# Optimization experiments

Measured on AMD Instinct MI355X. Metric: run time of the kernel, lower is better.

Reference implementation:

```python
import jax, jax.numpy as jnp
import numpy as np

K = 5
THRESHOLD = 0.1


def _l2norm(x, eps=1e-12):
    # matches torch.nn.functional.normalize(dim=-1)
    n = jnp.sqrt(jnp.sum(x * x, axis=-1, keepdims=True))
    return x / jnp.maximum(n, eps)


def setup_inputs() -> dict:
    key = jax.random.key(0)
    ks = jax.random.split(key, 5)
    B, CDD, HIS, L, LVL, H = 32, 5, 50, 32, 2, 256
    return {
        "cdd_repr": jax.random.normal(ks[0], (B, CDD, H), dtype=jnp.float32),
        "his_repr": jax.random.normal(ks[1], (B, HIS, H), dtype=jnp.float32),
        "his_embedding": jax.random.normal(ks[2], (B, HIS, L, LVL, H), dtype=jnp.float32),
        "his_attn_mask": jax.random.randint(ks[3], (B, HIS, L), 0, 2).astype(jnp.int32),
        # xavier-normal-ish init for the selection projection
        "W": jax.random.normal(ks[4], (H, H), dtype=jnp.float32) * np.float32(np.sqrt(2.0 / (H + H))),
        "b": jnp.zeros((H,), dtype=jnp.float32),
    }


def reference(cdd_repr, his_repr, his_embedding, his_attn_mask, W, b):
    # selection projection + L2 normalize
    c = _l2norm(cdd_repr @ W.T + b)           # [B, cdd, H]
    h = _l2norm(his_repr @ W.T + b)           # [B, his, H]
    # news-level attention scores
    attn = jnp.einsum("bcd,bhd->bch", c, h)   # [B, cdd, his]
    # top-k history selection (sorted descending, like torch.topk)
    vals, idx = jax.lax.top_k(attn, K)        # [B, cdd, k]
    # gather top-k history embeddings / masks per (batch, cdd)
    his_activated = jax.vmap(lambda e, i: e[i])(his_embedding, idx)   # [B, cdd, k, L, lvl, H]
    his_mask_activated = jax.vmap(lambda m, i: m[i])(his_attn_mask, idx)  # [B, cdd, k, L]
    # threshold mask + reweight (fused elementwise)
    w = jnp.where(vals < THRESHOLD, jnp.float32(0.0), vals)
    his_activated = his_activated * w[..., None, None, None]
    return his_activated, his_mask_activated
```

## Files before the change

kernel.cpp:

```cpp
#include <hip/hip_runtime.h>
#include <hip/hip_bf16.h>

#define B_    32
#define CDD_  5
#define HIS_  50
#define L_    32
#define LVL_  2
#define H_    256
#define K_    5
#define NCDD  (B_*CDD_)
#define NHIS  (B_*HIS_)
#define NROWS (NCDD + NHIS)
#define SLAB  (L_*LVL_*H_)
#define OUT0  ((size_t)NCDD*K_*SLAB)

__global__ __launch_bounds__(256) void proj_norm_kernel(
    const float* __restrict__ cdd, const float* __restrict__ his,
    const float* __restrict__ Wm, const float* __restrict__ bias,
    float* __restrict__ Y)
{
    __shared__ float xs[4][H_];
    __shared__ float part[4][4];
    __shared__ float inv[4];
    const int t = threadIdx.x;
    const int r0 = blockIdx.x * 4;

    {
        int rr = t >> 6, cc = t & 63;
        int row = r0 + rr;
        const float* src = (row < NCDD) ? (cdd + (size_t)row * H_)
                                        : (his + (size_t)(row - NCDD) * H_);
        ((float4*)xs[rr])[cc] = ((const float4*)src)[cc];
    }
    __syncthreads();

    float a0 = 0.f, a1 = 0.f, a2 = 0.f, a3 = 0.f;
    const float4* wrow = (const float4*)(Wm + (size_t)t * H_);
    #pragma unroll 8
    for (int c = 0; c < H_ / 4; ++c) {
        float4 wv = wrow[c];
        float4 x0 = ((float4*)xs[0])[c];
        float4 x1 = ((float4*)xs[1])[c];
        float4 x2 = ((float4*)xs[2])[c];
        float4 x3 = ((float4*)xs[3])[c];
        a0 += wv.x*x0.x + wv.y*x0.y + wv.z*x0.z + wv.w*x0.w;
        a1 += wv.x*x1.x + wv.y*x1.y + wv.z*x1.z + wv.w*x1.w;
        a2 += wv.x*x2.x + wv.y*x2.y + wv.z*x2.z + wv.w*x2.w;
        a3 += wv.x*x3.x + wv.y*x3.y + wv.z*x3.z + wv.w*x3.w;
    }
    const float bt = bias[t];
    float y0 = a0 + bt, y1 = a1 + bt, y2 = a2 + bt, y3 = a3 + bt;

    const int wave = t >> 6, lane = t & 63;
    float s0 = y0*y0, s1 = y1*y1, s2 = y2*y2, s3 = y3*y3;
    #pragma unroll
    for (int off = 32; off; off >>= 1) {
        s0 += __shfl_down(s0, off);
        s1 += __shfl_down(s1, off);
        s2 += __shfl_down(s2, off);
        s3 += __shfl_down(s3, off);
    }
    if (lane == 0) { part[0][wave] = s0; part[1][wave] = s1;
                     part[2][wave] = s2; part[3][wave] = s3; }
    __syncthreads();
    if (t < 4) {
        float s = part[t][0] + part[t][1] + part[t][2] + part[t][3];
        inv[t] = 1.0f / fmaxf(sqrtf(s), 1e-12f);
    }
    __syncthreads();

    float* yr = Y + (size_t)r0 * H_ + t;
    yr[0 * H_] = y0 * inv[0];
    yr[1 * H_] = y1 * inv[1];
    yr[2 * H_] = y2 * inv[2];
    yr[3 * H_] = y3 * inv[3];
}

__global__ __launch_bounds__(256) void attn_topk_kernel(
    const float* __restrict__ Y, const int* __restrict__ mask,
    int* __restrict__ idx_ws, float* __restrict__ w_ws,
    float* __restrict__ mask_out)
{
    const int bc = blockIdx.x;
    const int b  = bc / CDD_;
    __shared__ float cs[H_];
    __shared__ float scores[HIS_];
    __shared__ int   sidx[K_];
    const int t = threadIdx.x;

    cs[t] = Y[(size_t)bc * H_ + t];
    __syncthreads();

    const int wave = t >> 6, lane = t & 63;
    for (int h = wave; h < HIS_; h += 4) {
        const float4* hv = (const float4*)(Y + (size_t)(NCDD + b * HIS_ + h) * H_);
        float4 x  = hv[lane];
        float4 c4 = ((float4*)cs)[lane];
        float p = x.x*c4.x + x.y*c4.y + x.z*c4.z + x.w*c4.w;
        #pragma unroll
        for (int off = 32; off; off >>= 1) p += __shfl_down(p, off);
        if (lane == 0) scores[h] = p;
    }
    __syncthreads();

    if (t == 0) {
        #pragma unroll
        for (int k = 0; k < K_; ++k) {
            float best = -1e30f; int bi = 0;
            for (int h = 0; h < HIS_; ++h)
                if (scores[h] > best) { best = scores[h]; bi = h; }
            scores[bi] = -1e30f;
            sidx[k] = bi;
            idx_ws[bc * K_ + k] = bi;
            w_ws[bc * K_ + k]   = (best < 0.1f) ? 0.0f : best;
        }
    }
    __syncthreads();

    if (t < K_ * L_) {
        int k = t / L_, l = t % L_;
        mask_out[((size_t)bc * K_ + k) * L_ + l] =
            (float)mask[((size_t)(b * HIS_ + sidx[k])) * L_ + l];
    }
}

__global__ __launch_bounds__(256) void gather_scale_kernel(
    const float* __restrict__ emb, const int* __restrict__ idx_ws,
    const float* __restrict__ w_ws, float* __restrict__ out)
{
    const int gb    = blockIdx.x;
    const int slice = gb & 7;
    const int bck   = gb >> 3;
    const int bc    = bck / K_;
    const int b     = bc / CDD_;
    const int i     = idx_ws[bck];
    const float w   = w_ws[bck];

    const float4* src = (const float4*)(emb + (size_t)(b * HIS_ + i) * SLAB);
    float4*       dst = (float4*)(out + (size_t)bck * SLAB);
    const int base = slice * 512 + threadIdx.x;

    float4 v0 = src[base];
    float4 v1 = src[base + 256];
    v0.x *= w; v0.y *= w; v0.z *= w; v0.w *= w;
    v1.x *= w; v1.y *= w; v1.z *= w; v1.w *= w;
    dst[base]       = v0;
    dst[base + 256] = v1;
}

extern "C" void kernel_launch(void* const* d_in, const int* in_sizes, int n_in,
                              void* d_out, int out_size, void* d_ws, size_t ws_size,
                              hipStream_t stream) {
    const float* cdd  = (const float*)d_in[0];
    const float* his  = (const float*)d_in[1];
    const float* emb  = (const float*)d_in[2];
    const int*   mask = (const int*)  d_in[3];
    const float* Wm   = (const float*)d_in[4];
    const float* bias = (const float*)d_in[5];
    float* out = (float*)d_out;

    float* Y      = (float*)d_ws;
    int*   idx_ws = (int*)  ((char*)d_ws + (size_t)NROWS*H_*4);
    float* w_ws   = (float*)((char*)d_ws + (size_t)NROWS*H_*4 + 800*4);

    proj_norm_kernel<<<NROWS / 4, 256, 0, stream>>>(cdd, his, Wm, bias, Y);
    attn_topk_kernel<<<NCDD, 256, 0, stream>>>(Y, mask, idx_ws, w_ws, out + OUT0);
    gather_scale_kernel<<<NCDD * K_ * 8, 256, 0, stream>>>(emb, idx_ws, w_ws, out);
}
```

Baseline: 196.0 us.

## Transpose W for coalesced projection, skip gather loads for zero weights, nontemporal stores

Adds a kernel that transposes W so the projection kernel reads coalesced float4 rows of W^T, with each wave computing two rows and normalizing them via in-wave xor shuffles, which removes the block-level reductions and barriers. The gather kernel now uses fewer blocks, each handling four float4s per thread. It skips reading the embedding when the threshold weight is zero and writes zeros instead. Output writes use nontemporal stores to avoid polluting cache. This adds an extra kernel launch for the transpose.

```diff
diff --git a/kernel.cpp b/kernel.cpp
--- a/kernel.cpp
+++ b/kernel.cpp
@@ -14,19 +14,36 @@
 #define SLAB  (L_*LVL_*H_)
 #define OUT0  ((size_t)NCDD*K_*SLAB)
 
+typedef float f32x4 __attribute__((ext_vector_type(4)));
+
+__global__ __launch_bounds__(256) void transpose_w_kernel(
+    const float* __restrict__ Wm, float* __restrict__ WT)
+{
+    __shared__ float tile[64][65];
+    const int tx = threadIdx.x & 63, ty = threadIdx.x >> 6;
+    const int c0 = (blockIdx.x & 3) * 64, r0 = (blockIdx.x >> 2) * 64;
+    #pragma unroll
+    for (int i = 0; i < 16; ++i)
+        tile[ty + i*4][tx] = Wm[(size_t)(r0 + ty + i*4) * H_ + c0 + tx];
+    __syncthreads();
+    #pragma unroll
+    for (int i = 0; i < 16; ++i)
+        WT[(size_t)(c0 + ty + i*4) * H_ + r0 + tx] = tile[tx][ty + i*4];
+}
+
 __global__ __launch_bounds__(256) void proj_norm_kernel(
     const float* __restrict__ cdd, const float* __restrict__ his,
-    const float* __restrict__ Wm, const float* __restrict__ bias,
+    const float* __restrict__ WT, const float* __restrict__ bias,
     float* __restrict__ Y)
 {
-    __shared__ float xs[4][H_];
-    __shared__ float part[4][4];
-    __shared__ float inv[4];
+    __shared__ float xs[8][H_];
     const int t = threadIdx.x;
-    const int r0 = blockIdx.x * 4;
+    const int r0 = blockIdx.x * 8;
+    const int wave = t >> 6, lane = t & 63;
 
-    {
-        int rr = t >> 6, cc = t & 63;
+    #pragma unroll
+    for (int j = t; j < 8 * H_ / 4; j += 256) {
+        int rr = j >> 6, cc = j & 63;
         int row = r0 + rr;
         const float* src = (row < NCDD) ? (cdd + (size_t)row * H_)
                                         : (his + (size_t)(row - NCDD) * H_);
@@ -34,46 +51,35 @@
     }
     __syncthreads();
 
-    float a0 = 0.f, a1 = 0.f, a2 = 0.f, a3 = 0.f;
-    const float4* wrow = (const float4*)(Wm + (size_t)t * H_);
-    #pragma unroll 8
-    for (int c = 0; c < H_ / 4; ++c) {
-        float4 wv = wrow[c];
-        float4 x0 = ((float4*)xs[0])[c];
-        float4 x1 = ((float4*)xs[1])[c];
-        float4 x2 = ((float4*)xs[2])[c];
-        float4 x3 = ((float4*)xs[3])[c];
-        a0 += wv.x*x0.x + wv.y*x0.y + wv.z*x0.z + wv.w*x0.w;
-        a1 += wv.x*x1.x + wv.y*x1.y + wv.z*x1.z + wv.w*x1.w;
-        a2 += wv.x*x2.x + wv.y*x2.y + wv.z*x2.z + wv.w*x2.w;
-        a3 += wv.x*x3.x + wv.y*x3.y + wv.z*x3.z + wv.w*x3.w;
+    const int ra = 2 * wave, rb = ra + 1;
+    float4 a0 = {0,0,0,0}, a1 = {0,0,0,0};
+    #pragma unroll 4
+    for (int k = 0; k < H_; ++k) {
+        float4 wv = ((const float4*)(WT + (size_t)k * H_))[lane];
+        float x0 = xs[ra][k], x1 = xs[rb][k];
+        a0.x = fmaf(x0, wv.x, a0.x); a0.y = fmaf(x0, wv.y, a0.y);
+        a0.z = fmaf(x0, wv.z, a0.z); a0.w = fmaf(x0, wv.w, a0.w);
+        a1.x = fmaf(x1, wv.x, a1.x); a1.y = fmaf(x1, wv.y, a1.y);
+        a1.z = fmaf(x1, wv.z, a1.z); a1.w = fmaf(x1, wv.w, a1.w);
     }
-    const float bt = bias[t];
-    float y0 = a0 + bt, y1 = a1 + bt, y2 = a2 + bt, y3 = a3 + bt;
+    float4 bv = ((const float4*)bias)[lane];
+    a0.x += bv.x; a0.y += bv.y; a0.z += bv.z; a0.w += bv.w;
+    a1.x += bv.x; a1.y += bv.y; a1.z += bv.z; a1.w += bv.w;
 
-    const int wave = t >> 6, lane = t & 63;
-    float s0 = y0*y0, s1 = y1*y1, s2 = y2*y2, s3 = y3*y3;
+    float s0 = a0.x*a0.x + a0.y*a0.y + a0.z*a0.z + a0.w*a0.w;
+    float s1 = a1.x*a1.x + a1.y*a1.y + a1.z*a1.z + a1.w*a1.w;
     #pragma unroll
-    for (int off = 32; off; off >>= 1) {
-        s0 += __shfl_down(s0, off);
-        s1 += __shfl_down(s1, off);
-        s2 += __shfl_down(s2, off);
-        s3 += __shfl_down(s3, off);
+    for (int off = 1; off < 64; off <<= 1) {
+        s0 += __shfl_xor(s0, off);
+        s1 += __shfl_xor(s1, off);
     }
-    if (lane == 0) { part[0][wave] = s0; part[1][wave] = s1;
-                     part[2][wave] = s2; part[3][wave] = s3; }
-    __syncthreads();
-    if (t < 4) {
-        float s = part[t][0] + part[t][1] + part[t][2] + part[t][3];
-        inv[t] = 1.0f / fmaxf(sqrtf(s), 1e-12f);
-    }
-    __syncthreads();
+    float i0 = 1.0f / fmaxf(sqrtf(s0), 1e-12f);
+    float i1 = 1.0f / fmaxf(sqrtf(s1), 1e-12f);
+    a0.x *= i0; a0.y *= i0; a0.z *= i0; a0.w *= i0;
+    a1.x *= i1; a1.y *= i1; a1.z *= i1; a1.w *= i1;
 
-    float* yr = Y + (size_t)r0 * H_ + t;
-    yr[0 * H_] = y0 * inv[0];
-    yr[1 * H_] = y1 * inv[1];
-    yr[2 * H_] = y2 * inv[2];
-    yr[3 * H_] = y3 * inv[3];
+    ((float4*)(Y + (size_t)(r0 + ra) * H_))[lane] = a0;
+    ((float4*)(Y + (size_t)(r0 + rb) * H_))[lane] = a1;
 }
 
 __global__ __launch_bounds__(256) void attn_topk_kernel(
@@ -128,24 +134,33 @@
     const float* __restrict__ emb, const int* __restrict__ idx_ws,
     const float* __restrict__ w_ws, float* __restrict__ out)
 {
-    const int gb    = blockIdx.x;
-    const int slice = gb & 7;
-    const int bck   = gb >> 3;
-    const int bc    = bck / K_;
-    const int b     = bc / CDD_;
-    const int i     = idx_ws[bck];
-    const float w   = w_ws[bck];
+    const int gb   = blockIdx.x;
+    const int part = gb & 3;
+    const int bck  = gb >> 2;
+    const int bc   = bck / K_;
+    const int b    = bc / CDD_;
+    const float w  = w_ws[bck];
 
-    const float4* src = (const float4*)(emb + (size_t)(b * HIS_ + i) * SLAB);
-    float4*       dst = (float4*)(out + (size_t)bck * SLAB);
-    const int base = slice * 512 + threadIdx.x;
+    f32x4* dst = (f32x4*)((float4*)(out + (size_t)bck * SLAB) + part * 1024 + threadIdx.x);
 
-    float4 v0 = src[base];
-    float4 v1 = src[base + 256];
-    v0.x *= w; v0.y *= w; v0.z *= w; v0.w *= w;
-    v1.x *= w; v1.y *= w; v1.z *= w; v1.w *= w;
-    dst[base]       = v0;
-    dst[base + 256] = v1;
+    if (w == 0.0f) {
+        f32x4 z = {0.f, 0.f, 0.f, 0.f};
+        #pragma unroll
+        for (int j = 0; j < 4; ++j)
+            __builtin_nontemporal_store(z, dst + j * 256);
+    } else {
+        const int i = idx_ws[bck];
+        const f32x4* src = (const f32x4*)((const float4*)(emb + (size_t)(b * HIS_ + i) * SLAB)
+                          + part * 1024 + threadIdx.x);
+        f32x4 v[4];
+        #pragma unroll
+        for (int j = 0; j < 4; ++j) v[j] = src[j * 256];
+        #pragma unroll
+        for (int j = 0; j < 4; ++j) {
+            v[j] *= w;
+            __builtin_nontemporal_store(v[j], dst + j * 256);
+        }
+    }
 }
 
 extern "C" void kernel_launch(void* const* d_in, const int* in_sizes, int n_in,
@@ -159,11 +174,13 @@
     const float* bias = (const float*)d_in[5];
     float* out = (float*)d_out;
 
-    float* Y      = (float*)d_ws;
-    int*   idx_ws = (int*)  ((char*)d_ws + (size_t)NROWS*H_*4);
-    float* w_ws   = (float*)((char*)d_ws + (size_t)NROWS*H_*4 + 800*4);
+    float* WT     = (float*)d_ws;
+    float* Y      = WT + (size_t)H_ * H_;
+    int*   idx_ws = (int*)(Y + (size_t)NROWS * H_);
+    float* w_ws   = (float*)(idx_ws + NCDD * K_);
 
-    proj_norm_kernel<<<NROWS / 4, 256, 0, stream>>>(cdd, his, Wm, bias, Y);
+    transpose_w_kernel<<<16, 256, 0, stream>>>(Wm, WT);
+    proj_norm_kernel<<<NROWS / 8, 256, 0, stream>>>(cdd, his, WT, bias, Y);
     attn_topk_kernel<<<NCDD, 256, 0, stream>>>(Y, mask, idx_ws, w_ws, out + OUT0);
-    gather_scale_kernel<<<NCDD * K_ * 8, 256, 0, stream>>>(emb, idx_ws, w_ws, out);
+    gather_scale_kernel<<<NCDD * K_ * 4, 256, 0, stream>>>(emb, idx_ws, w_ws, out);
 }
```

After: 203.7 us. 1.04x slower.
